# Performance work log

Hardware: AMD Instinct MI355X
Metric: run time of the kernel (lower is better)

## Reference

```python
import jax, jax.numpy as jnp
import numpy as np

HIDDEN = 2048
INTER = 8192
RETRIEVAL = 128
NUM_EXPERTS = 4096
NUM_KEYS = 64  # sqrt(NUM_EXPERTS)
TOP_K = 8
B, S = 4, 2048


def setup_inputs() -> dict:
    key = jax.random.key(0)
    ks = jax.random.split(key, 8)
    sc = 0.02
    return {
        "hidden_states": jax.random.normal(ks[0], (B, S, HIDDEN), jnp.float32),
        "W_q": jax.random.normal(ks[1], (HIDDEN, RETRIEVAL), jnp.float32) * sc,
        "keys": jax.random.normal(ks[2], (2, RETRIEVAL // 2, NUM_KEYS), jnp.float32) * sc,
        "down_embed": jax.random.normal(ks[3], (NUM_EXPERTS, HIDDEN), jnp.float32) * sc,
        "up_embed": jax.random.normal(ks[4], (NUM_EXPERTS, HIDDEN), jnp.float32) * sc,
        "gate_w": jax.random.normal(ks[5], (HIDDEN, INTER), jnp.float32) * sc,
        "up_w": jax.random.normal(ks[6], (HIDDEN, INTER), jnp.float32) * sc,
        "down_w": jax.random.normal(ks[7], (INTER, HIDDEN), jnp.float32) * sc,
    }


def reference(hidden_states, W_q, keys, down_embed, up_embed, gate_w, up_w, down_w):
    b, s, h = hidden_states.shape
    n = b * s
    # product-key routing (faithful to the source's view(2, N, -1) reshape)
    queries = (hidden_states @ W_q).reshape(2, n, RETRIEVAL // 2)  # [2, N, rd/2]
    routing = jnp.einsum('tnd,tdk->tnk', queries, keys)            # [2, N, num_keys]
    scores2, idx2 = jax.lax.top_k(routing, TOP_K)                  # [2, N, k]
    sx, sy = scores2[0], scores2[1]
    ix, iy = idx2[0], idx2[1]
    all_scores = (sx[:, :, None] + sy[:, None, :]).reshape(n, TOP_K * TOP_K)
    all_idx = (ix[:, :, None] * NUM_KEYS + iy[:, None, :]).reshape(n, TOP_K * TOP_K)
    scores, pk = jax.lax.top_k(all_scores, TOP_K)                  # [N, k]
    indices = jnp.take_along_axis(all_idx, pk, axis=-1)            # [N, k]
    # expert embedding gather + per-token tiny matmuls
    de = down_embed[indices]                                       # [N, k, H]
    ue = up_embed[indices]                                         # [N, k, H]
    x = hidden_states.reshape(n, h)
    ew = jnp.einsum('nh,nkh->nk', x, de)                           # [N, k]
    ew = jax.nn.silu(ew) * jax.nn.softmax(scores, axis=-1)
    experts_states = jnp.einsum('nk,nkh->nh', ew, ue).reshape(b, s, h)
    # dense SwiGLU MLP branch
    mlp = (jax.nn.silu(x @ gate_w) * (x @ up_w)) @ down_w
    return mlp.reshape(b, s, h) + experts_states
```

## Files before the change

### kernel.cpp

```cpp
#include <hip/hip_runtime.h>
#include <cstdint>
#include <cstddef>

#define HIDDEN 2048
#define INTER 8192
#define NTOK 8192
#define RET 128
#define NKEYS 64
#define TOPK 8

typedef __bf16 bf16_t;
typedef bf16_t bf16x8 __attribute__((ext_vector_type(8)));
typedef float floatx4 __attribute__((ext_vector_type(4)));

__device__ inline unsigned short f2bf(float f) {
  union { float f; unsigned u; } v; v.f = f;
  unsigned r = v.u + 0x7FFFu + ((v.u >> 16) & 1u);
  return (unsigned short)(r >> 16);
}
__device__ inline float bf2f(unsigned short s) {
  union { unsigned u; float f; } v; v.u = ((unsigned)s) << 16;
  return v.f;
}

__device__ inline void gld_lds16(unsigned short* lds, const unsigned short* g) {
  auto* l3 = reinterpret_cast<__attribute__((address_space(3))) unsigned int*>(
      reinterpret_cast<uintptr_t>(lds));
  auto* g1 = reinterpret_cast<const __attribute__((address_space(1))) unsigned int*>(
      reinterpret_cast<uintptr_t>(g));
  __builtin_amdgcn_global_load_lds(g1, l3, 16, 0, 0);
}

__global__ __launch_bounds__(256) void cvt_bf16(const float* __restrict__ in,
                                                unsigned short* __restrict__ out,
                                                int count4) {
  for (int i = blockIdx.x * blockDim.x + threadIdx.x; i < count4;
       i += gridDim.x * blockDim.x) {
    float4 v = reinterpret_cast<const float4*>(in)[i];
    ushort4 o;
    o.x = f2bf(v.x); o.y = f2bf(v.y); o.z = f2bf(v.z); o.w = f2bf(v.w);
    reinterpret_cast<ushort4*>(out)[i] = o;
  }
}

__global__ __launch_bounds__(256) void transpose_cvt(const float* __restrict__ in,
                                                     unsigned short* __restrict__ out,
                                                     int R, int C) {
  __shared__ float tile[32][33];
  int c0 = blockIdx.x * 32, r0 = blockIdx.y * 32;
  int tx = threadIdx.x, ty = threadIdx.y;
#pragma unroll
  for (int it = 0; it < 4; ++it)
    tile[ty + it * 8][tx] = in[(size_t)(r0 + ty + it * 8) * C + c0 + tx];
  __syncthreads();
#pragma unroll
  for (int it = 0; it < 4; ++it)
    out[(size_t)(c0 + ty + it * 8) * R + r0 + tx] = f2bf(tile[tx][ty + it * 8]);
}

enum { EPI_F32 = 0, EPI_BF16 = 1, EPI_SILU = 2, EPI_ADDF32 = 3 };

template <int MODE>
__global__ __launch_bounds__(256) void gemm_bt(const unsigned short* __restrict__ A,
                                               const unsigned short* __restrict__ B,
                                               float* __restrict__ Cf,
                                               unsigned short* __restrict__ Cb,
                                               int M, int N, int K) {
  __shared__ unsigned short As[128 * 64];
  __shared__ unsigned short Bs[128 * 64];
  const int tid = threadIdx.x;
  const int lane = tid & 63, wid = tid >> 6;
  const int wm = wid >> 1, wn = wid & 1;

  int bx = blockIdx.x, by = blockIdx.y;
  if ((gridDim.x & 15) == 0 && (gridDim.y & 15) == 0) {
    int lin = by * gridDim.x + bx;
    int stW = gridDim.x >> 4;
    int st = lin >> 8;
    int wi = lin & 255;
    bx = (st % stW) * 16 + (wi & 15);
    by = (st / stW) * 16 + (wi >> 4);
  }
  const int m0 = by * 128, n0 = bx * 128;
  const int lr = lane & 15, q = lane >> 4;
  const int swz = lr & 7;

  floatx4 acc[4][4];
#pragma unroll
  for (int i = 0; i < 4; ++i)
#pragma unroll
    for (int j = 0; j < 4; ++j) acc[i][j] = (floatx4){0.f, 0.f, 0.f, 0.f};

  for (int k0 = 0; k0 < K; k0 += 64) {
#pragma unroll
    for (int s = 0; s < 4; ++s) {
      int c = s * 256 + wid * 64 + lane;
      int row = c >> 3, cc = (c & 7) ^ (row & 7);
      gld_lds16(&As[(s * 256 + wid * 64) * 8],
                A + (size_t)(m0 + row) * K + k0 + cc * 8);
      gld_lds16(&Bs[(s * 256 + wid * 64) * 8],
                B + (size_t)(n0 + row) * K + k0 + cc * 8);
    }
    __syncthreads();
#pragma unroll
    for (int kc = 0; kc < 2; ++kc) {
      const int coff = ((kc * 4 + q) ^ swz) * 8;
      bf16x8 af[4], bfv[4];
#pragma unroll
      for (int t = 0; t < 4; ++t) {
        af[t] = *reinterpret_cast<const bf16x8*>(
            &As[(wm * 64 + t * 16 + lr) * 64 + coff]);
        bfv[t] = *reinterpret_cast<const bf16x8*>(
            &Bs[(wn * 64 + t * 16 + lr) * 64 + coff]);
      }
#pragma unroll
      for (int i = 0; i < 4; ++i)
#pragma unroll
        for (int j = 0; j < 4; ++j)
          acc[i][j] = __builtin_amdgcn_mfma_f32_16x16x32_bf16(af[i], bfv[j],
                                                              acc[i][j], 0, 0, 0);
    }
    __syncthreads();
  }

#pragma unroll
  for (int i = 0; i < 4; ++i) {
    int rbase = m0 + wm * 64 + i * 16 + q * 4;
#pragma unroll
    for (int j = 0; j < 4; ++j) {
      int col = n0 + wn * 64 + j * 16 + lr;
#pragma unroll
      for (int r = 0; r < 4; ++r) {
        size_t idx = (size_t)(rbase + r) * N + col;
        float v = acc[i][j][r];
        if (MODE == EPI_F32) {
          Cf[idx] = v;
        } else if (MODE == EPI_BF16) {
          Cb[idx] = f2bf(v);
        } else if (MODE == EPI_SILU) {
          float g = bf2f(Cb[idx]);
          float sg = g / (1.f + __expf(-g));
          Cb[idx] = f2bf(sg * v);
        } else {
          Cf[idx] = v + Cf[idx];
        }
      }
    }
  }
}

__global__ __launch_bounds__(256) void routing_kernel(const float* __restrict__ Q,
                                                      const float* __restrict__ keys,
                                                      int* __restrict__ topi,
                                                      float* __restrict__ topw) {
  __shared__ float k0s[64 * 64];
  __shared__ float k1s[64 * 64];
  for (int i = threadIdx.x; i < 64 * 64; i += 256) {
    k0s[i] = keys[i];
    k1s[i] = keys[64 * 64 + i];
  }
  __syncthreads();
  const int lane = threadIdx.x & 63, wid = threadIdx.x >> 6;
  const int gw = blockIdx.x * 4 + wid;
  const float NEG = -__builtin_inff();

  for (int n = gw; n < NTOK; n += 1024) {
    int cbase = (n & 1) * 64;
    float qx = Q[(size_t)(n >> 1) * RET + cbase + lane];
    float qy = Q[(size_t)(NTOK / 2 + (n >> 1)) * RET + cbase + lane];
    float rx = 0.f, ry = 0.f;
#pragma unroll 8
    for (int d = 0; d < 64; ++d) {
      rx += __shfl(qx, d) * k0s[d * 64 + lane];
      ry += __shfl(qy, d) * k1s[d * 64 + lane];
    }
    float mvx = rx, mvy = ry;
    float keptx = 0.f, kepty = 0.f;
    int keptix = 0, keptiy = 0;
#pragma unroll
    for (int a = 0; a < 8; ++a) {
      float v = mvx; int ii = lane;
#pragma unroll
      for (int off = 32; off; off >>= 1) {
        float ov = __shfl_xor(v, off); int oi = __shfl_xor(ii, off);
        if (ov > v || (ov == v && oi < ii)) { v = ov; ii = oi; }
      }
      if (lane == a) { keptx = v; keptix = ii; }
      if (lane == ii) mvx = NEG;
      float w = mvy; int jj = lane;
#pragma unroll
      for (int off = 32; off; off >>= 1) {
        float ow = __shfl_xor(w, off); int oj = __shfl_xor(jj, off);
        if (ow > w || (ow == w && oj < jj)) { w = ow; jj = oj; }
      }
      if (lane == a) { kepty = w; keptiy = jj; }
      if (lane == jj) mvy = NEG;
    }
    float sa = __shfl(keptx, lane >> 3), sb = __shfl(kepty, lane & 7);
    int ia = __shfl(keptix, lane >> 3), ib = __shfl(keptiy, lane & 7);
    float mv = sa + sb;
    int pe = ia * NKEYS + ib;
    float maxs = 0.f, denom = 0.f, kw = 0.f;
    int ke = 0;
#pragma unroll
    for (int a = 0; a < 8; ++a) {
      float v = mv; int pos = lane; int e = pe;
#pragma unroll
      for (int off = 32; off; off >>= 1) {
        float ov = __shfl_xor(v, off);
        int opos = __shfl_xor(pos, off);
        int oe = __shfl_xor(e, off);
        if (ov > v || (ov == v && opos < pos)) { v = ov; pos = opos; e = oe; }
      }
      if (a == 0) maxs = v;
      denom += __expf(v - maxs);
      if (lane == a) { kw = __expf(v - maxs); ke = e; }
      if (lane == pos) mv = NEG;
    }
    if (lane < 8) {
      topw[(size_t)n * 8 + lane] = kw / denom;
      topi[(size_t)n * 8 + lane] = ke;
    }
  }
}

__global__ __launch_bounds__(256) void expert_kernel(const float* __restrict__ X,
                                                     const float* __restrict__ de,
                                                     const float* __restrict__ ue,
                                                     const int* __restrict__ topi,
                                                     const float* __restrict__ topw,
                                                     float* __restrict__ out) {
  const int n = blockIdx.x, t = threadIdx.x;
  __shared__ float red[4];
  __shared__ float coef_s;
  __shared__ int eidx[8];
  __shared__ float ewt[8];
  if (t < 8) {
    eidx[t] = topi[(size_t)n * 8 + t];
    ewt[t] = topw[(size_t)n * 8 + t];
  }
  const float* x = X + (size_t)n * HIDDEN + t * 8;
  float4 x0 = *(const float4*)x, x1 = *(const float4*)(x + 4);
  float a0 = 0, a1 = 0, a2 = 0, a3 = 0, a4 = 0, a5 = 0, a6 = 0, a7 = 0;
  __syncthreads();
#pragma unroll
  for (int k = 0; k < 8; ++k) {
    const float* dr = de + (size_t)eidx[k] * HIDDEN + t * 8;
    float4 d0 = *(const float4*)dr, d1 = *(const float4*)(dr + 4);
    float p = x0.x * d0.x + x0.y * d0.y + x0.z * d0.z + x0.w * d0.w +
              x1.x * d1.x + x1.y * d1.y + x1.z * d1.z + x1.w * d1.w;
#pragma unroll
    for (int off = 32; off; off >>= 1) p += __shfl_xor(p, off);
    if ((t & 63) == 0) red[t >> 6] = p;
    __syncthreads();
    if (t == 0) {
      float s = red[0] + red[1] + red[2] + red[3];
      coef_s = (s / (1.f + expf(-s))) * ewt[k];
    }
    __syncthreads();
    float c = coef_s;
    const float* ur = ue + (size_t)eidx[k] * HIDDEN + t * 8;
    float4 u0 = *(const float4*)ur, u1 = *(const float4*)(ur + 4);
    a0 += c * u0.x; a1 += c * u0.y; a2 += c * u0.z; a3 += c * u0.w;
    a4 += c * u1.x; a5 += c * u1.y; a6 += c * u1.z; a7 += c * u1.w;
  }
  float* op = out + (size_t)n * HIDDEN + t * 8;
  *(float4*)op = make_float4(a0, a1, a2, a3);
  *(float4*)(op + 4) = make_float4(a4, a5, a6, a7);
}

extern "C" void kernel_launch(void* const* d_in, const int* in_sizes, int n_in,
                              void* d_out, int out_size, void* d_ws, size_t ws_size,
                              hipStream_t stream) {
  const float* X    = (const float*)d_in[0];
  const float* Wq   = (const float*)d_in[1];
  const float* keys = (const float*)d_in[2];
  const float* de   = (const float*)d_in[3];
  const float* ue   = (const float*)d_in[4];
  const float* Wg   = (const float*)d_in[5];
  const float* Wu   = (const float*)d_in[6];
  const float* Wd   = (const float*)d_in[7];
  float* out = (float*)d_out;

  char* ws = (char*)d_ws;
  size_t o = 0;
  unsigned short* xb  = (unsigned short*)(ws + o); o += (size_t)NTOK * HIDDEN * 2;
  unsigned short* wgt = (unsigned short*)(ws + o); o += (size_t)HIDDEN * INTER * 2;
  unsigned short* wut = (unsigned short*)(ws + o); o += (size_t)HIDDEN * INTER * 2;
  unsigned short* wdt = (unsigned short*)(ws + o); o += (size_t)HIDDEN * INTER * 2;
  unsigned short* hbuf= (unsigned short*)(ws + o); o += (size_t)NTOK * INTER * 2;
  unsigned short* wqt = (unsigned short*)(ws + o); o += (size_t)RET * HIDDEN * 2;
  float* Q            = (float*)(ws + o);          o += (size_t)NTOK * RET * 4;
  int* topi           = (int*)(ws + o);            o += (size_t)NTOK * TOPK * 4;
  float* topw         = (float*)(ws + o);          o += (size_t)NTOK * TOPK * 4;

  cvt_bf16<<<4096, 256, 0, stream>>>(X, xb, NTOK * HIDDEN / 4);
  transpose_cvt<<<dim3(INTER / 32, HIDDEN / 32), dim3(32, 8), 0, stream>>>(Wg, wgt, HIDDEN, INTER);
  transpose_cvt<<<dim3(INTER / 32, HIDDEN / 32), dim3(32, 8), 0, stream>>>(Wu, wut, HIDDEN, INTER);
  transpose_cvt<<<dim3(HIDDEN / 32, INTER / 32), dim3(32, 8), 0, stream>>>(Wd, wdt, INTER, HIDDEN);
  transpose_cvt<<<dim3(RET / 32, HIDDEN / 32), dim3(32, 8), 0, stream>>>(Wq, wqt, HIDDEN, RET);

  gemm_bt<EPI_F32><<<dim3(1, NTOK / 128), 256, 0, stream>>>(xb, wqt, Q, nullptr,
                                                            NTOK, RET, HIDDEN);
  routing_kernel<<<256, 256, 0, stream>>>(Q, keys, topi, topw);
  expert_kernel<<<NTOK, 256, 0, stream>>>(X, de, ue, topi, topw, out);

  gemm_bt<EPI_BF16><<<dim3(INTER / 128, NTOK / 128), 256, 0, stream>>>(
      xb, wgt, nullptr, hbuf, NTOK, INTER, HIDDEN);
  gemm_bt<EPI_SILU><<<dim3(INTER / 128, NTOK / 128), 256, 0, stream>>>(
      xb, wut, nullptr, hbuf, NTOK, INTER, HIDDEN);
  gemm_bt<EPI_ADDF32><<<dim3(HIDDEN / 128, NTOK / 128), 256, 0, stream>>>(
      hbuf, wdt, out, nullptr, NTOK, HIDDEN, INTER);
}
```

Before: 1.736 ms.

## Fuse gate and up GEMMs into one kernel with SiLU epilogue, remap blocks per XCD

Replaces the two separate gate and up GEMMs with a single kernel that loads each A tile once, computes both gate and up accumulators, and applies SiLU times up in the epilogue. This removes one full re-read of the activation matrix, the bf16 round trip of the gate output through memory, and one kernel launch. The block swizzle is also changed from 16x16 supertiles to an XCD-aware mapping with snake ordering, aiming for better L2 reuse per chiplet. The fused kernel uses twice the accumulator registers and extra LDS, which may limit occupancy (launch bounds request two blocks per SM).

```diff
diff --git a/kernel.cpp b/kernel.cpp
--- a/kernel.cpp
+++ b/kernel.cpp
@@ -29,6 +29,18 @@
   auto* g1 = reinterpret_cast<const __attribute__((address_space(1))) unsigned int*>(
       reinterpret_cast<uintptr_t>(g));
   __builtin_amdgcn_global_load_lds(g1, l3, 16, 0, 0);
+}
+
+__device__ inline void xcd_map(int gx, int gy, int& bx, int& by) {
+  if ((gx & 7) != 0) return;
+  int lin = by * gx + bx;
+  int W = gx >> 3;
+  int xcd = lin & 7;
+  int j = lin >> 3;
+  int r = j / W, c = j % W;
+  if (r & 1) c = W - 1 - c;
+  bx = xcd * W + c;
+  by = r;
 }
 
 __global__ __launch_bounds__(256) void cvt_bf16(const float* __restrict__ in,
@@ -58,29 +70,20 @@
     out[(size_t)(c0 + ty + it * 8) * R + r0 + tx] = f2bf(tile[tx][ty + it * 8]);
 }
 
-enum { EPI_F32 = 0, EPI_BF16 = 1, EPI_SILU = 2, EPI_ADDF32 = 3 };
+enum { EPI_F32 = 0, EPI_ADDF32 = 3 };
 
 template <int MODE>
 __global__ __launch_bounds__(256) void gemm_bt(const unsigned short* __restrict__ A,
                                                const unsigned short* __restrict__ B,
                                                float* __restrict__ Cf,
-                                               unsigned short* __restrict__ Cb,
                                                int M, int N, int K) {
   __shared__ unsigned short As[128 * 64];
   __shared__ unsigned short Bs[128 * 64];
   const int tid = threadIdx.x;
   const int lane = tid & 63, wid = tid >> 6;
   const int wm = wid >> 1, wn = wid & 1;
-
   int bx = blockIdx.x, by = blockIdx.y;
-  if ((gridDim.x & 15) == 0 && (gridDim.y & 15) == 0) {
-    int lin = by * gridDim.x + bx;
-    int stW = gridDim.x >> 4;
-    int st = lin >> 8;
-    int wi = lin & 255;
-    bx = (st % stW) * 16 + (wi & 15);
-    by = (st / stW) * 16 + (wi >> 4);
-  }
+  xcd_map(gridDim.x, gridDim.y, bx, by);
   const int m0 = by * 128, n0 = bx * 128;
   const int lr = lane & 15, q = lane >> 4;
   const int swz = lr & 7;
@@ -133,17 +136,87 @@
       for (int r = 0; r < 4; ++r) {
         size_t idx = (size_t)(rbase + r) * N + col;
         float v = acc[i][j][r];
-        if (MODE == EPI_F32) {
-          Cf[idx] = v;
-        } else if (MODE == EPI_BF16) {
-          Cb[idx] = f2bf(v);
-        } else if (MODE == EPI_SILU) {
-          float g = bf2f(Cb[idx]);
-          float sg = g / (1.f + __expf(-g));
-          Cb[idx] = f2bf(sg * v);
-        } else {
-          Cf[idx] = v + Cf[idx];
+        if (MODE == EPI_F32) Cf[idx] = v;
+        else Cf[idx] = v + Cf[idx];
+      }
+    }
+  }
+}
+
+__global__ __launch_bounds__(256, 2) void gemm_gateup(
+    const unsigned short* __restrict__ A, const unsigned short* __restrict__ Bg,
+    const unsigned short* __restrict__ Bu, unsigned short* __restrict__ H,
+    int M, int N, int K) {
+  __shared__ unsigned short As[128 * 64];
+  __shared__ unsigned short Bgs[128 * 64];
+  __shared__ unsigned short Bus[128 * 64];
+  const int tid = threadIdx.x;
+  const int lane = tid & 63, wid = tid >> 6;
+  const int wm = wid >> 1, wn = wid & 1;
+  int bx = blockIdx.x, by = blockIdx.y;
+  xcd_map(gridDim.x, gridDim.y, bx, by);
+  const int m0 = by * 128, n0 = bx * 128;
+  const int lr = lane & 15, q = lane >> 4;
+  const int swz = lr & 7;
+
+  floatx4 accg[4][4], accu[4][4];
+#pragma unroll
+  for (int i = 0; i < 4; ++i)
+#pragma unroll
+    for (int j = 0; j < 4; ++j) {
+      accg[i][j] = (floatx4){0.f, 0.f, 0.f, 0.f};
+      accu[i][j] = (floatx4){0.f, 0.f, 0.f, 0.f};
+    }
+
+  for (int k0 = 0; k0 < K; k0 += 64) {
+#pragma unroll
+    for (int s = 0; s < 4; ++s) {
+      int c = s * 256 + wid * 64 + lane;
+      int row = c >> 3, cc = (c & 7) ^ (row & 7);
+      size_t arow = (size_t)(m0 + row) * K + k0 + cc * 8;
+      size_t brow = (size_t)(n0 + row) * K + k0 + cc * 8;
+      gld_lds16(&As[(s * 256 + wid * 64) * 8], A + arow);
+      gld_lds16(&Bgs[(s * 256 + wid * 64) * 8], Bg + brow);
+      gld_lds16(&Bus[(s * 256 + wid * 64) * 8], Bu + brow);
+    }
+    __syncthreads();
+#pragma unroll
+    for (int kc = 0; kc < 2; ++kc) {
+      const int coff = ((kc * 4 + q) ^ swz) * 8;
+      bf16x8 af[4], bgf[4], buf[4];
+#pragma unroll
+      for (int t = 0; t < 4; ++t) {
+        af[t] = *reinterpret_cast<const bf16x8*>(
+            &As[(wm * 64 + t * 16 + lr) * 64 + coff]);
+        bgf[t] = *reinterpret_cast<const bf16x8*>(
+            &Bgs[(wn * 64 + t * 16 + lr) * 64 + coff]);
+        buf[t] = *reinterpret_cast<const bf16x8*>(
+            &Bus[(wn * 64 + t * 16 + lr) * 64 + coff]);
+      }
+#pragma unroll
+      for (int i = 0; i < 4; ++i)
+#pragma unroll
+        for (int j = 0; j < 4; ++j) {
+          accg[i][j] = __builtin_amdgcn_mfma_f32_16x16x32_bf16(af[i], bgf[j],
+                                                               accg[i][j], 0, 0, 0);
+          accu[i][j] = __builtin_amdgcn_mfma_f32_16x16x32_bf16(af[i], buf[j],
+                                                               accu[i][j], 0, 0, 0);
         }
+    }
+    __syncthreads();
+  }
+
+#pragma unroll
+  for (int i = 0; i < 4; ++i) {
+    int rbase = m0 + wm * 64 + i * 16 + q * 4;
+#pragma unroll
+    for (int j = 0; j < 4; ++j) {
+      int col = n0 + wn * 64 + j * 16 + lr;
+#pragma unroll
+      for (int r = 0; r < 4; ++r) {
+        float g = accg[i][j][r];
+        float h = (g / (1.f + __expf(-g))) * accu[i][j][r];
+        H[(size_t)(rbase + r) * N + col] = f2bf(h);
       }
     }
   }
@@ -300,15 +373,13 @@
   transpose_cvt<<<dim3(HIDDEN / 32, INTER / 32), dim3(32, 8), 0, stream>>>(Wd, wdt, INTER, HIDDEN);
   transpose_cvt<<<dim3(RET / 32, HIDDEN / 32), dim3(32, 8), 0, stream>>>(Wq, wqt, HIDDEN, RET);
 
-  gemm_bt<EPI_F32><<<dim3(1, NTOK / 128), 256, 0, stream>>>(xb, wqt, Q, nullptr,
+  gemm_bt<EPI_F32><<<dim3(1, NTOK / 128), 256, 0, stream>>>(xb, wqt, Q,
                                                             NTOK, RET, HIDDEN);
   routing_kernel<<<256, 256, 0, stream>>>(Q, keys, topi, topw);
   expert_kernel<<<NTOK, 256, 0, stream>>>(X, de, ue, topi, topw, out);
 
-  gemm_bt<EPI_BF16><<<dim3(INTER / 128, NTOK / 128), 256, 0, stream>>>(
-      xb, wgt, nullptr, hbuf, NTOK, INTER, HIDDEN);
-  gemm_bt<EPI_SILU><<<dim3(INTER / 128, NTOK / 128), 256, 0, stream>>>(
-      xb, wut, nullptr, hbuf, NTOK, INTER, HIDDEN);
+  gemm_gateup<<<dim3(INTER / 128, NTOK / 128), 256, 0, stream>>>(
+      xb, wgt, wut, hbuf, NTOK, INTER, HIDDEN);
   gemm_bt<EPI_ADDF32><<<dim3(HIDDEN / 128, NTOK / 128), 256, 0, stream>>>(
-      hbuf, wdt, out, nullptr, NTOK, HIDDEN, INTER);
-}
+      hbuf, wdt, out, NTOK, HIDDEN, INTER);
+}
```

New measurement: 1.560 ms. 1.11x faster.
